# Kernel optimization log

Measured on AMD Instinct MI355X. Metric: run time of the kernel, lower is better.

Reference implementation:

```python
import jax, jax.numpy as jnp
import numpy as np

TEMPERATURE = 0.5

def setup_inputs() -> dict:
    key = jax.random.key(0)
    k1, k2 = jax.random.split(key)
    N, D = 4096, 256
    return {
        "z_i": jax.random.normal(k1, (N, D), dtype=jnp.float32),
        "z_j": jax.random.normal(k2, (N, D), dtype=jnp.float32),
    }

def reference(z_i, z_j):
    N = z_i.shape[0]
    z = jnp.concatenate([z_i, z_j], axis=0)                      # [2N, D]
    # cosine similarity via normalize + GEMM (same math as broadcasted CosineSimilarity)
    zn = z / jnp.linalg.norm(z, axis=-1, keepdims=True)
    sim = (zn @ zn.T) / TEMPERATURE                              # [2N, 2N]
    twoN = 2 * N
    eye = jnp.eye(twoN, dtype=bool)
    labels = jnp.arange(N, dtype=jnp.int32)
    labels = jnp.concatenate([labels, labels])
    pos_mask = (labels[None, :] == labels[:, None]) & (~eye)     # positive pairs, no diagonal
    # removing the diagonal before exp == zeroing exp on the diagonal
    exps = jnp.where(eye, 0.0, jnp.exp(sim))                     # [2N, 2N]
    pos = jnp.sum(jnp.where(pos_mask, exps, 0.0), axis=1)        # [2N]
    denom = jnp.sum(exps, axis=1)                                # [2N]
    loss = -jnp.mean(jnp.log(pos / denom))
    return loss
```

## Files before the change

kernel.cpp:

```cpp
#include <hip/hip_runtime.h>
#include <hip/hip_bf16.h>

#define TWO_N 8192
#define NHALF 4096
#define D 256
#define NTILE 64
#define BLK_ELEMS 32768
static constexpr float INV_T = 2.0f;

typedef __attribute__((ext_vector_type(8))) short short8;
typedef __attribute__((ext_vector_type(4))) float f32x4;

#define AS1 __attribute__((address_space(1)))
#define AS3 __attribute__((address_space(3)))

__device__ __forceinline__ ushort f2bfu(float f) {
    __hip_bfloat16 b = __float2bfloat16(f);
    return *reinterpret_cast<ushort*>(&b);
}

__global__ __launch_bounds__(256) void norm_pos_kernel(
        const float* __restrict__ z_i, const float* __restrict__ z_j,
        ushort* __restrict__ znb, float* __restrict__ sim_pos,
        float* __restrict__ denom) {
    const int wid = threadIdx.x >> 6, lane = threadIdx.x & 63;
    const int i = blockIdx.x * 4 + wid;
    const float4 vi = *reinterpret_cast<const float4*>(z_i + (size_t)i * D + lane * 4);
    const float4 vj = *reinterpret_cast<const float4*>(z_j + (size_t)i * D + lane * 4);
    float ssi = vi.x * vi.x + vi.y * vi.y + vi.z * vi.z + vi.w * vi.w;
    float ssj = vj.x * vj.x + vj.y * vj.y + vj.z * vj.z + vj.w * vj.w;
    float dt  = vi.x * vj.x + vi.y * vj.y + vi.z * vj.z + vi.w * vj.w;
    #pragma unroll
    for (int off = 32; off; off >>= 1) {
        ssi += __shfl_xor(ssi, off);
        ssj += __shfl_xor(ssj, off);
        dt  += __shfl_xor(dt,  off);
    }
    const float ri = rsqrtf(ssi), rj = rsqrtf(ssj);
    ushort4 oi, oj;
    oi.x = f2bfu(vi.x * ri); oi.y = f2bfu(vi.y * ri);
    oi.z = f2bfu(vi.z * ri); oi.w = f2bfu(vi.w * ri);
    oj.x = f2bfu(vj.x * rj); oj.y = f2bfu(vj.y * rj);
    oj.z = f2bfu(vj.z * rj); oj.w = f2bfu(vj.w * rj);
    const int c = lane >> 1, e = (lane & 1) * 4;
    const int i2 = i + NHALF;
    const size_t bi = ((size_t)(i  >> 7) * 32 + c) * 1024 + (i  & 127) * 8 + e;
    const size_t bj = ((size_t)(i2 >> 7) * 32 + c) * 1024 + (i2 & 127) * 8 + e;
    *reinterpret_cast<ushort4*>(znb + bi) = oi;
    *reinterpret_cast<ushort4*>(znb + bj) = oj;
    if (lane == 0) {
        const float sp = dt * ri * rj * INV_T;
        sim_pos[i] = sp;
        sim_pos[i + NHALF] = sp;
        denom[i] = 0.0f;
        denom[i + NHALF] = 0.0f;
    }
}

__global__ __launch_bounds__(256) void gemm_denom_kernel(
        const ushort* __restrict__ znb, float* __restrict__ denom) {
    const int tr = blockIdx.x;
    const int tc = blockIdx.y;
    if (tc < tr) return;

    __shared__ ushort As[3][4 * 128 * 8];
    __shared__ ushort Bs[3][4 * 128 * 8];

    const int tid  = threadIdx.x;
    const int lane = tid & 63;
    const int wid  = tid >> 6;
    const int wr   = wid >> 1;
    const int wc   = wid & 1;
    const int r16  = lane & 15;
    const int kgrp = lane >> 4;
    const int row0 = tr * 128;
    const int col0 = tc * 128;

    const ushort* gA = znb + (size_t)tr * BLK_ELEMS + tid * 8;
    const ushort* gB = znb + (size_t)tc * BLK_ELEMS + tid * 8;
    const int d0 = (0 * 256 + wid * 64) * 8;
    const int d1 = (1 * 256 + wid * 64) * 8;

    #define STAGE(buf, koff)                                                      \
        do {                                                                      \
            __builtin_amdgcn_global_load_lds((const AS1 void*)(gA + (koff)),      \
                (AS3 void*)(As[buf] + d0), 16, 0, 0);                             \
            __builtin_amdgcn_global_load_lds((const AS1 void*)(gA + (koff) + 2048),\
                (AS3 void*)(As[buf] + d1), 16, 0, 0);                             \
            __builtin_amdgcn_global_load_lds((const AS1 void*)(gB + (koff)),      \
                (AS3 void*)(Bs[buf] + d0), 16, 0, 0);                             \
            __builtin_amdgcn_global_load_lds((const AS1 void*)(gB + (koff) + 2048),\
                (AS3 void*)(Bs[buf] + d1), 16, 0, 0);                             \
        } while (0)

    f32x4 acc[4][4];
    #pragma unroll
    for (int m = 0; m < 4; ++m)
        #pragma unroll
        for (int n = 0; n < 4; ++n) {
            f32x4 z = {0.f, 0.f, 0.f, 0.f};
            acc[m][n] = z;
        }

    STAGE(0, 0);
    STAGE(1, 4096);

    #pragma unroll
    for (int ks = 0; ks < 8; ++ks) {
        const int cur = ks % 3;
        if (ks < 7) asm volatile("s_waitcnt vmcnt(4)" ::: "memory");
        else        asm volatile("s_waitcnt vmcnt(0)" ::: "memory");
        __builtin_amdgcn_s_barrier();
        asm volatile("" ::: "memory");
        if (ks < 6) STAGE((ks + 2) % 3, (ks + 2) * 4096);
        short8 a[4], b[4];
        #pragma unroll
        for (int m = 0; m < 4; ++m)
            a[m] = *reinterpret_cast<const short8*>(
                As[cur] + ((kgrp * 128) + wr * 64 + m * 16 + r16) * 8);
        #pragma unroll
        for (int n = 0; n < 4; ++n)
            b[n] = *reinterpret_cast<const short8*>(
                Bs[cur] + ((kgrp * 128) + wc * 64 + n * 16 + r16) * 8);
        #pragma unroll
        for (int m = 0; m < 4; ++m)
            #pragma unroll
            for (int n = 0; n < 4; ++n)
                acc[m][n] = __builtin_amdgcn_mfma_f32_16x16x32_bf16(
                    a[m], b[n], acc[m][n], 0, 0, 0);
    }
    #undef STAGE

    const bool offdiag = (tr != tc);
    float cs[4] = {0.f, 0.f, 0.f, 0.f};
    #pragma unroll
    for (int m = 0; m < 4; ++m) {
        #pragma unroll
        for (int reg = 0; reg < 4; ++reg) {
            const int rg = row0 + wr * 64 + m * 16 + kgrp * 4 + reg;
            float rs = 0.f;
            #pragma unroll
            for (int n = 0; n < 4; ++n) {
                const int cg = col0 + wc * 64 + n * 16 + r16;
                float e = __expf(acc[m][n][reg] * INV_T);
                if (rg == cg) e = 0.f;
                rs += e;
                cs[n] += e;
            }
            rs += __shfl_xor(rs, 1);
            rs += __shfl_xor(rs, 2);
            rs += __shfl_xor(rs, 4);
            rs += __shfl_xor(rs, 8);
            if (r16 == 0) atomicAdd(&denom[rg], rs);
        }
    }
    if (offdiag) {
        #pragma unroll
        for (int n = 0; n < 4; ++n) {
            cs[n] += __shfl_xor(cs[n], 16);
            cs[n] += __shfl_xor(cs[n], 32);
        }
        if (kgrp == 0) {
            #pragma unroll
            for (int n = 0; n < 4; ++n)
                atomicAdd(&denom[col0 + wc * 64 + n * 16 + r16], cs[n]);
        }
    }
}

__global__ __launch_bounds__(1024) void final_kernel(
        const float* __restrict__ sim_pos, const float* __restrict__ denom,
        float* __restrict__ out) {
    const int tid = threadIdx.x;
    float s = 0.f;
    for (int i = tid; i < TWO_N; i += 1024)
        s += sim_pos[i] - logf(denom[i]);
    #pragma unroll
    for (int off = 32; off; off >>= 1) s += __shfl_down(s, off);
    __shared__ float red[16];
    const int wid = tid >> 6, lane = tid & 63;
    if (lane == 0) red[wid] = s;
    __syncthreads();
    if (tid == 0) {
        float t = 0.f;
        #pragma unroll
        for (int w = 0; w < 16; ++w) t += red[w];
        out[0] = -t / (float)TWO_N;
    }
}

extern "C" void kernel_launch(void* const* d_in, const int* in_sizes, int n_in,
                              void* d_out, int out_size, void* d_ws, size_t ws_size,
                              hipStream_t stream) {
    const float* z_i = (const float*)d_in[0];
    const float* z_j = (const float*)d_in[1];
    float* out = (float*)d_out;

    ushort* znb     = (ushort*)d_ws;
    float*  sim_pos = (float*)((char*)d_ws + (size_t)TWO_N * D * 2);
    float*  denom   = sim_pos + TWO_N;

    norm_pos_kernel<<<NHALF / 4, 256, 0, stream>>>(z_i, z_j, znb, sim_pos, denom);
    dim3 grid(NTILE, NTILE);
    gemm_denom_kernel<<<grid, 256, 0, stream>>>(znb, denom);
    final_kernel<<<1, 1024, 0, stream>>>(sim_pos, denom, out);
}
```

Measured before the change: 54.63 us.

## Load GEMM operands directly from global memory instead of LDS staging

Drops the triple-buffered global-to-LDS async staging and its barriers from the similarity GEMM. Each wave now loads its A and B fragments straight from the pre-tiled bf16 buffer in global memory into registers. This removes the LDS traffic and per-k-step barriers, but every fragment is now fetched separately by each wave that needs it, relying on L1/L2 for reuse. The loss of explicit prefetch may also expose global load latency to the MFMA loop.

```diff
diff --git a/kernel.cpp b/kernel.cpp
--- a/kernel.cpp
+++ b/kernel.cpp
@@ -10,9 +10,6 @@
 
 typedef __attribute__((ext_vector_type(8))) short short8;
 typedef __attribute__((ext_vector_type(4))) float f32x4;
-
-#define AS1 __attribute__((address_space(1)))
-#define AS3 __attribute__((address_space(3)))
 
 __device__ __forceinline__ ushort f2bfu(float f) {
     __hip_bfloat16 b = __float2bfloat16(f);
@@ -63,9 +60,6 @@
     const int tc = blockIdx.y;
     if (tc < tr) return;
 
-    __shared__ ushort As[3][4 * 128 * 8];
-    __shared__ ushort Bs[3][4 * 128 * 8];
-
     const int tid  = threadIdx.x;
     const int lane = tid & 63;
     const int wid  = tid >> 6;
@@ -76,22 +70,8 @@
     const int row0 = tr * 128;
     const int col0 = tc * 128;
 
-    const ushort* gA = znb + (size_t)tr * BLK_ELEMS + tid * 8;
-    const ushort* gB = znb + (size_t)tc * BLK_ELEMS + tid * 8;
-    const int d0 = (0 * 256 + wid * 64) * 8;
-    const int d1 = (1 * 256 + wid * 64) * 8;
-
-    #define STAGE(buf, koff)                                                      \
-        do {                                                                      \
-            __builtin_amdgcn_global_load_lds((const AS1 void*)(gA + (koff)),      \
-                (AS3 void*)(As[buf] + d0), 16, 0, 0);                             \
-            __builtin_amdgcn_global_load_lds((const AS1 void*)(gA + (koff) + 2048),\
-                (AS3 void*)(As[buf] + d1), 16, 0, 0);                             \
-            __builtin_amdgcn_global_load_lds((const AS1 void*)(gB + (koff)),      \
-                (AS3 void*)(Bs[buf] + d0), 16, 0, 0);                             \
-            __builtin_amdgcn_global_load_lds((const AS1 void*)(gB + (koff) + 2048),\
-                (AS3 void*)(Bs[buf] + d1), 16, 0, 0);                             \
-        } while (0)
+    const ushort* pA = znb + (size_t)tr * BLK_ELEMS + kgrp * 1024 + (wr * 64 + r16) * 8;
+    const ushort* pB = znb + (size_t)tc * BLK_ELEMS + kgrp * 1024 + (wc * 64 + r16) * 8;
 
     f32x4 acc[4][4];
     #pragma unroll
@@ -102,26 +82,15 @@
             acc[m][n] = z;
         }
 
-    STAGE(0, 0);
-    STAGE(1, 4096);
-
     #pragma unroll
     for (int ks = 0; ks < 8; ++ks) {
-        const int cur = ks % 3;
-        if (ks < 7) asm volatile("s_waitcnt vmcnt(4)" ::: "memory");
-        else        asm volatile("s_waitcnt vmcnt(0)" ::: "memory");
-        __builtin_amdgcn_s_barrier();
-        asm volatile("" ::: "memory");
-        if (ks < 6) STAGE((ks + 2) % 3, (ks + 2) * 4096);
         short8 a[4], b[4];
         #pragma unroll
         for (int m = 0; m < 4; ++m)
-            a[m] = *reinterpret_cast<const short8*>(
-                As[cur] + ((kgrp * 128) + wr * 64 + m * 16 + r16) * 8);
+            a[m] = *reinterpret_cast<const short8*>(pA + ks * 4096 + m * 128);
         #pragma unroll
         for (int n = 0; n < 4; ++n)
-            b[n] = *reinterpret_cast<const short8*>(
-                Bs[cur] + ((kgrp * 128) + wc * 64 + n * 16 + r16) * 8);
+            b[n] = *reinterpret_cast<const short8*>(pB + ks * 4096 + n * 128);
         #pragma unroll
         for (int m = 0; m < 4; ++m)
             #pragma unroll
@@ -129,7 +98,6 @@
                 acc[m][n] = __builtin_amdgcn_mfma_f32_16x16x32_bf16(
                     a[m], b[n], acc[m][n], 0, 0, 0);
     }
-    #undef STAGE
 
     const bool offdiag = (tr != tc);
     float cs[4] = {0.f, 0.f, 0.f, 0.f};
```

After: 58.86 us. 7.8% more time.

## Make triangular GEMM persistent with cross-tile prefetch of next tile

Applied to the files above, without the earlier changes.

Replaces the 64x64 grid, where blocks below the diagonal exit early, with a persistent grid of 768 blocks. Each block walks the 2080 upper-triangular tiles in strided order, decoding row and column with a loop. The last two pipeline stages prefetch the first K-slices of the next tile, so that load overlaps the exp and atomic epilogue of the current tile. The cost is a full vmcnt(0) drain at the end of each tile, per-tile index decode loops, and a fixed persistent count that may not match the CU count well.

```diff
diff --git a/kernel.cpp b/kernel.cpp
--- a/kernel.cpp
+++ b/kernel.cpp
@@ -5,6 +5,8 @@
 #define NHALF 4096
 #define D 256
 #define NTILE 64
+#define NTRI  2080
+#define NPERS 768
 #define BLK_ELEMS 32768
 static constexpr float INV_T = 2.0f;
 
@@ -59,10 +61,6 @@
 
 __global__ __launch_bounds__(256) void gemm_denom_kernel(
         const ushort* __restrict__ znb, float* __restrict__ denom) {
-    const int tr = blockIdx.x;
-    const int tc = blockIdx.y;
-    if (tc < tr) return;
-
     __shared__ ushort As[3][4 * 128 * 8];
     __shared__ ushort Bs[3][4 * 128 * 8];
 
@@ -73,99 +71,126 @@
     const int wc   = wid & 1;
     const int r16  = lane & 15;
     const int kgrp = lane >> 4;
-    const int row0 = tr * 128;
-    const int col0 = tc * 128;
+    const int d0 = (0 * 256 + wid * 64) * 8;
+    const int d1 = (1 * 256 + wid * 64) * 8;
+
+    int tr = 0, rem = (int)blockIdx.x;
+    while (rem >= NTILE - tr) { rem -= NTILE - tr; ++tr; }
+    int tc = tr + rem;
 
     const ushort* gA = znb + (size_t)tr * BLK_ELEMS + tid * 8;
     const ushort* gB = znb + (size_t)tc * BLK_ELEMS + tid * 8;
-    const int d0 = (0 * 256 + wid * 64) * 8;
-    const int d1 = (1 * 256 + wid * 64) * 8;
-
-    #define STAGE(buf, koff)                                                      \
+
+    #define STG(buf, pA, pB, koff)                                                \
         do {                                                                      \
-            __builtin_amdgcn_global_load_lds((const AS1 void*)(gA + (koff)),      \
+            __builtin_amdgcn_global_load_lds((const AS1 void*)((pA) + (koff)),    \
                 (AS3 void*)(As[buf] + d0), 16, 0, 0);                             \
-            __builtin_amdgcn_global_load_lds((const AS1 void*)(gA + (koff) + 2048),\
+            __builtin_amdgcn_global_load_lds((const AS1 void*)((pA) + (koff) + 2048), \
                 (AS3 void*)(As[buf] + d1), 16, 0, 0);                             \
-            __builtin_amdgcn_global_load_lds((const AS1 void*)(gB + (koff)),      \
+            __builtin_amdgcn_global_load_lds((const AS1 void*)((pB) + (koff)),    \
                 (AS3 void*)(Bs[buf] + d0), 16, 0, 0);                             \
-            __builtin_amdgcn_global_load_lds((const AS1 void*)(gB + (koff) + 2048),\
+            __builtin_amdgcn_global_load_lds((const AS1 void*)((pB) + (koff) + 2048), \
                 (AS3 void*)(Bs[buf] + d1), 16, 0, 0);                             \
         } while (0)
 
-    f32x4 acc[4][4];
-    #pragma unroll
-    for (int m = 0; m < 4; ++m)
-        #pragma unroll
-        for (int n = 0; n < 4; ++n) {
-            f32x4 z = {0.f, 0.f, 0.f, 0.f};
-            acc[m][n] = z;
-        }
-
-    STAGE(0, 0);
-    STAGE(1, 4096);
-
-    #pragma unroll
-    for (int ks = 0; ks < 8; ++ks) {
-        const int cur = ks % 3;
-        if (ks < 7) asm volatile("s_waitcnt vmcnt(4)" ::: "memory");
-        else        asm volatile("s_waitcnt vmcnt(0)" ::: "memory");
-        __builtin_amdgcn_s_barrier();
-        asm volatile("" ::: "memory");
-        if (ks < 6) STAGE((ks + 2) % 3, (ks + 2) * 4096);
-        short8 a[4], b[4];
+    STG(0, gA, gB, 0);
+    STG(1, gA, gB, 4096);
+    int ph = 0;
+
+    for (int tile = (int)blockIdx.x; tile < NTRI; tile += NPERS) {
+        const bool hasNext = (tile + NPERS) < NTRI;
+        int tr2 = tr, tc2 = tc;
+        const ushort *gA2 = gA, *gB2 = gB;
+        if (hasNext) {
+            int r2 = tile + NPERS;
+            tr2 = 0;
+            while (r2 >= NTILE - tr2) { r2 -= NTILE - tr2; ++tr2; }
+            tc2 = tr2 + r2;
+            gA2 = znb + (size_t)tr2 * BLK_ELEMS + tid * 8;
+            gB2 = znb + (size_t)tc2 * BLK_ELEMS + tid * 8;
+        }
+        const int row0 = tr * 128;
+        const int col0 = tc * 128;
+
+        f32x4 acc[4][4];
         #pragma unroll
         for (int m = 0; m < 4; ++m)
-            a[m] = *reinterpret_cast<const short8*>(
-                As[cur] + ((kgrp * 128) + wr * 64 + m * 16 + r16) * 8);
-        #pragma unroll
-        for (int n = 0; n < 4; ++n)
-            b[n] = *reinterpret_cast<const short8*>(
-                Bs[cur] + ((kgrp * 128) + wc * 64 + n * 16 + r16) * 8);
-        #pragma unroll
-        for (int m = 0; m < 4; ++m)
+            #pragma unroll
+            for (int n = 0; n < 4; ++n) {
+                f32x4 z = {0.f, 0.f, 0.f, 0.f};
+                acc[m][n] = z;
+            }
+
+        #pragma unroll
+        for (int ks = 0; ks < 8; ++ks) {
+            const int cur  = (ph + ks) % 3;
+            const int nbuf = (ph + ks + 2) % 3;
+            if (ks == 7 && !hasNext) asm volatile("s_waitcnt vmcnt(0)" ::: "memory");
+            else                     asm volatile("s_waitcnt vmcnt(4)" ::: "memory");
+            __builtin_amdgcn_s_barrier();
+            asm volatile("" ::: "memory");
+            if (ks < 6)       STG(nbuf, gA,  gB,  (ks + 2) * 4096);
+            else if (hasNext) STG(nbuf, gA2, gB2, (ks - 6) * 4096);
+            short8 a[4], b[4];
+            #pragma unroll
+            for (int m = 0; m < 4; ++m)
+                a[m] = *reinterpret_cast<const short8*>(
+                    As[cur] + ((kgrp * 128) + wr * 64 + m * 16 + r16) * 8);
             #pragma unroll
             for (int n = 0; n < 4; ++n)
-                acc[m][n] = __builtin_amdgcn_mfma_f32_16x16x32_bf16(
-                    a[m], b[n], acc[m][n], 0, 0, 0);
-    }
-    #undef STAGE
-
-    const bool offdiag = (tr != tc);
-    float cs[4] = {0.f, 0.f, 0.f, 0.f};
-    #pragma unroll
-    for (int m = 0; m < 4; ++m) {
-        #pragma unroll
-        for (int reg = 0; reg < 4; ++reg) {
-            const int rg = row0 + wr * 64 + m * 16 + kgrp * 4 + reg;
-            float rs = 0.f;
+                b[n] = *reinterpret_cast<const short8*>(
+                    Bs[cur] + ((kgrp * 128) + wc * 64 + n * 16 + r16) * 8);
+            #pragma unroll
+            for (int m = 0; m < 4; ++m)
+                #pragma unroll
+                for (int n = 0; n < 4; ++n)
+                    acc[m][n] = __builtin_amdgcn_mfma_f32_16x16x32_bf16(
+                        a[m], b[n], acc[m][n], 0, 0, 0);
+        }
+        ph = (ph + 2) % 3;
+
+        const bool offdiag = (tr != tc);
+        float cs[4] = {0.f, 0.f, 0.f, 0.f};
+        #pragma unroll
+        for (int m = 0; m < 4; ++m) {
+            #pragma unroll
+            for (int reg = 0; reg < 4; ++reg) {
+                const int rg = row0 + wr * 64 + m * 16 + kgrp * 4 + reg;
+                float rs = 0.f;
+                #pragma unroll
+                for (int n = 0; n < 4; ++n) {
+                    const int cg = col0 + wc * 64 + n * 16 + r16;
+                    float e = __expf(acc[m][n][reg] * INV_T);
+                    if (rg == cg) e = 0.f;
+                    rs += e;
+                    cs[n] += e;
+                }
+                rs += __shfl_xor(rs, 1);
+                rs += __shfl_xor(rs, 2);
+                rs += __shfl_xor(rs, 4);
+                rs += __shfl_xor(rs, 8);
+                if (r16 == 0) atomicAdd(&denom[rg], rs);
+            }
+        }
+        if (offdiag) {
             #pragma unroll
             for (int n = 0; n < 4; ++n) {
-                const int cg = col0 + wc * 64 + n * 16 + r16;
-                float e = __expf(acc[m][n][reg] * INV_T);
-                if (rg == cg) e = 0.f;
-                rs += e;
-                cs[n] += e;
-            }
-            rs += __shfl_xor(rs, 1);
-            rs += __shfl_xor(rs, 2);
-            rs += __shfl_xor(rs, 4);
-            rs += __shfl_xor(rs, 8);
-            if (r16 == 0) atomicAdd(&denom[rg], rs);
-        }
-    }
-    if (offdiag) {
-        #pragma unroll
-        for (int n = 0; n < 4; ++n) {
-            cs[n] += __shfl_xor(cs[n], 16);
-            cs[n] += __shfl_xor(cs[n], 32);
-        }
-        if (kgrp == 0) {
-            #pragma unroll
-            for (int n = 0; n < 4; ++n)
-                atomicAdd(&denom[col0 + wc * 64 + n * 16 + r16], cs[n]);
-        }
-    }
+                cs[n] += __shfl_xor(cs[n], 16);
+                cs[n] += __shfl_xor(cs[n], 32);
+            }
+            if (kgrp == 0) {
+                #pragma unroll
+                for (int n = 0; n < 4; ++n)
+                    atomicAdd(&denom[col0 + wc * 64 + n * 16 + r16], cs[n]);
+            }
+        }
+
+        if (hasNext) {
+            asm volatile("s_waitcnt vmcnt(0)" ::: "memory");
+        }
+        tr = tr2; tc = tc2; gA = gA2; gB = gB2;
+    }
+    #undef STG
 }
 
 __global__ __launch_bounds__(1024) void final_kernel(
@@ -196,12 +221,11 @@
     const float* z_j = (const float*)d_in[1];
     float* out = (float*)d_out;
 
-    ushort* znb     = (ushort*)d_ws;
-    float*  sim_pos = (float*)((char*)d_ws + (size_t)TWO_N * D * 2);
-    float*  denom   = sim_pos + TWO_N;
+    ushort* znb      = (ushort*)d_ws;
+    float*  sim_pos  = (float*)((char*)d_ws + (size_t)TWO_N * D * 2);
+    float*  denom    = sim_pos + TWO_N;
 
     norm_pos_kernel<<<NHALF / 4, 256, 0, stream>>>(z_i, z_j, znb, sim_pos, denom);
-    dim3 grid(NTILE, NTILE);
-    gemm_denom_kernel<<<grid, 256, 0, stream>>>(znb, denom);
+    gemm_denom_kernel<<<NPERS, 256, 0, stream>>>(znb, denom);
     final_kernel<<<1, 1024, 0, stream>>>(sim_pos, denom, out);
 }
```

Measured after the change: 78.17 us. 1.43x slower.
